# Performance work log

Measured on AMD Instinct MI355X. Metric: run time of the kernel, lower is better.

## Reference

```python
import jax, jax.numpy as jnp
import numpy as np

N, D = 8192, 64
DC_PERCENTILE = 2.0  # np.percentile(distance_matrix, 2)


def setup_inputs() -> dict:
    key = jax.random.key(0)
    data = jax.random.normal(key, (N, D), dtype=jnp.float32)
    return {
        "data": data,
        "rho_threshold": jnp.float32(0.5),
        "delta_threshold": jnp.float32(0.5),
    }


def _cluster(data, rho_t, delta_t):
    n = data.shape[0]
    # pairwise Euclidean distances via GEMM: ||xi||^2 + ||xj||^2 - 2 xi.xj
    sq = jnp.sum(data * data, axis=1)
    d2 = sq[:, None] + sq[None, :] - 2.0 * (data @ data.T)
    dist = jnp.sqrt(jnp.maximum(d2, 0.0))  # [n, n]

    dc = jnp.percentile(dist, DC_PERCENTILE)
    # local density rho_i = sum_j exp(-(d_ij/dc)^2)
    rho = jnp.sum(jnp.exp(-(dist / dc) ** 2), axis=1)  # [n]

    # delta_i = min dist to any point with strictly higher density
    higher = rho[None, :] > rho[:, None]  # [n, n] bool
    masked = jnp.where(higher, dist, jnp.inf)
    delta_m = jnp.min(masked, axis=1)
    nhd_m = jnp.argmin(masked, axis=1)
    has_higher = jnp.any(higher, axis=1)
    delta = jnp.where(has_higher, delta_m, jnp.max(dist, axis=1))
    nhd = jnp.where(has_higher, nhd_m, jnp.arange(n))  # nearest higher-density idx

    # cluster centers: rho and delta above thresholds; label = rank among centers
    is_center = (rho > rho_t) & (delta > delta_t)
    center_rank = jnp.cumsum(is_center.astype(jnp.int32)) - 1
    labels0 = jnp.where(is_center, center_rank, -1).astype(jnp.int32)

    # propagate labels in order of decreasing density (stable argsort, as numpy subset order)
    order = jnp.argsort(-rho)

    def step(labels, i):
        lab = jnp.where(labels[i] < 0, labels[nhd[i]], labels[i])
        return labels.at[i].set(lab), None

    labels, _ = jax.lax.scan(step, labels0, order)
    return labels


def reference(data, rho_threshold, delta_threshold):
    return _cluster(data, rho_threshold, delta_threshold)
```

## Files before the change

kernel.cpp:

```cpp
#include <hip/hip_runtime.h>
#include <stdint.h>

typedef unsigned int u32;
typedef unsigned long long u64;

#define NPTS 8192
#define NTRI 2080
#define NSLICE 16u

#define WS_HIST    0u
#define WS_STATE   524288u
#define WS_DC      524320u
#define WS_SQ      524800u
#define WS_ROWMAX  557568u
#define WS_RHOD    590336u
#define WS_MINKEY  655872u
#define WS_CAND    721408u
#define CAP        32768u
#define WS_S       1048576ull

#define K_RANK 1342177u

__device__ __forceinline__ u64 umin64(u64 a, u64 b) { return a < b ? a : b; }

__device__ __forceinline__ void tri_decode(int t, int& bi, int& bj) {
  int a = (int)((sqrtf(8.0f * (float)t + 1.0f) - 1.0f) * 0.5f);
  while ((a + 1) * (a + 2) / 2 <= t) ++a;
  while (a * (a + 1) / 2 > t) --a;
  int b = t - a * (a + 1) / 2;
  bi = 63 - a; bj = 63 - b;
}

__device__ __forceinline__ u32 bin_of(float d2v) {
  float kf = fminf(d2v * 1048576.0f, 2147483520.0f);
  return min(((u32)kf) >> 15, 8191u);
}

__device__ __forceinline__ u32 block_exscan_1024(u32 v, u32* aux, u32& total) {
  const int lane = threadIdx.x & 63, wave = threadIdx.x >> 6;
  u32 inc = v;
#pragma unroll
  for (int m = 1; m < 64; m <<= 1) {
    u32 o = (u32)__shfl_up((int)inc, m, 64);
    if (lane >= m) inc += o;
  }
  if (lane == 63) aux[wave] = inc;
  __syncthreads();
  if (wave == 0) {
    u32 wv = (lane < 16) ? aux[lane] : 0u;
    u32 winc = wv;
#pragma unroll
    for (int m = 1; m < 16; m <<= 1) {
      u32 o = (u32)__shfl_up((int)winc, m, 64);
      if (lane >= m) winc += o;
    }
    if (lane < 16) aux[16 + lane] = winc - wv;
    if (lane == 15) aux[33] = winc;
  }
  __syncthreads();
  total = aux[33];
  return aux[16 + wave] + (inc - v);
}

__device__ __forceinline__ void tile128(
    const float* __restrict__ X, const float* __restrict__ sq,
    float (*As)[132], float (*Bs)[132],
    int bi, int bj, int tx, int ty, float (&d2)[8][8])
{
  const int tid = threadIdx.x;
  const float4* Xv = reinterpret_cast<const float4*>(X);
  float acc[8][8] = {};
  for (int ph = 0; ph < 2; ++ph) {
    if (ph) __syncthreads();
#pragma unroll
    for (int rep = 0; rep < 4; ++rep) {
      int idx = rep * 256 + tid;
      int i   = idx >> 3;
      int q   = idx & 7;
      int col = (((i >> 2) ^ (q >> 1)) << 2) | (i & 3);
      float4 va = Xv[(bi * 128 + i) * 16 + ph * 8 + q];
      As[4*q+0][col] = va.x; As[4*q+1][col] = va.y; As[4*q+2][col] = va.z; As[4*q+3][col] = va.w;
      float4 vb = Xv[(bj * 128 + i) * 16 + ph * 8 + q];
      Bs[4*q+0][col] = vb.x; Bs[4*q+1][col] = vb.y; Bs[4*q+2][col] = vb.z; Bs[4*q+3][col] = vb.w;
    }
    __syncthreads();
#pragma unroll
    for (int c8 = 0; c8 < 4; ++c8) {
#pragma unroll
      for (int u = 0; u < 8; ++u) {
        int k = c8 * 8 + u;
        float4 a0 = *reinterpret_cast<const float4*>(&As[k][((2*ty+0) ^ c8) << 2]);
        float4 a1 = *reinterpret_cast<const float4*>(&As[k][((2*ty+1) ^ c8) << 2]);
        float4 b0 = *reinterpret_cast<const float4*>(&Bs[k][((2*tx+0) ^ c8) << 2]);
        float4 b1 = *reinterpret_cast<const float4*>(&Bs[k][((2*tx+1) ^ c8) << 2]);
        float a[8] = {a0.x,a0.y,a0.z,a0.w,a1.x,a1.y,a1.z,a1.w};
        float b[8] = {b0.x,b0.y,b0.z,b0.w,b1.x,b1.y,b1.z,b1.w};
#pragma unroll
        for (int r = 0; r < 8; ++r)
#pragma unroll
          for (int c = 0; c < 8; ++c)
            acc[r][c] = fmaf(a[r], b[c], acc[r][c]);
      }
    }
  }
  float sqa[8], sqb[8];
#pragma unroll
  for (int r = 0; r < 8; ++r) sqa[r] = sq[bi * 128 + ty * 8 + r];
#pragma unroll
  for (int c = 0; c < 8; ++c) sqb[c] = sq[bj * 128 + tx * 8 + c];
#pragma unroll
  for (int r = 0; r < 8; ++r)
#pragma unroll
    for (int c = 0; c < 8; ++c)
      d2[r][c] = fmaxf((sqa[r] + sqb[c]) - 2.0f * acc[r][c], 0.0f);
}


__device__ __forceinline__ void collect_body(
    float (&d2)[8][8], int bi, int bj, int tx, int ty, u32* __restrict__ ws)
{
  u32* st = ws + WS_STATE / 4;
  const u32 b0 = st[0], b1 = st[1];
  u32* ctr = st + 4;
  u64* cand = reinterpret_cast<u64*>((char*)ws + WS_CAND);
  const int ig0 = bi * 128 + ty * 8, jg0 = bj * 128 + tx * 8;
  const bool offd = (bi < bj);
  const int lane = threadIdx.x & 63;
#pragma unroll
  for (int r = 0; r < 8; ++r)
#pragma unroll
    for (int c = 0; c < 8; ++c) {
      int ig = ig0 + r, jg = jg0 + c;
      u32 w = offd ? 2u : (ig < jg ? 2u : (ig == jg ? 1u : 0u));
      u32 bin = bin_of(d2[r][c]);
      bool ic = w && (bin == b0 || bin == b1);
      u64 m = __ballot(ic);
      if (m) {
        int leader = __ffsll((long long)m) - 1;
        u32 base = 0;
        if (lane == leader) base = atomicAdd(ctr, (u32)__popcll(m));
        base = (u32)__shfl((int)base, leader);
        if (ic) {
          u32 pos = base + (u32)__popcll(m & ((1ull << lane) - 1ull));
          if (pos < CAP)
            cand[pos] = (((u64)__float_as_uint(d2[r][c])) << 32) | (u64)w;
        }
      }
    }
}

__device__ __forceinline__ void rho_body(
    float (&d2)[8][8], int bi, int bj, int tx, int ty, u32* __restrict__ ws)
{
  __shared__ double redB[4][128];
  const int tid = threadIdx.x;
  const int wv = tid >> 6, lane = tid & 63;
  const float dcf = *reinterpret_cast<const float*>((const char*)ws + WS_DC);
  const float inv2 = 1.0f / (dcf * dcf);
  const int ig0 = bi * 128 + ty * 8, jg0 = bj * 128 + tx * 8;
  const bool diag = (bi == bj);
  float rA[8] = {}, rB[8] = {};
#pragma unroll
  for (int r = 0; r < 8; ++r)
#pragma unroll
    for (int c = 0; c < 8; ++c) {
      float t = __expf(-(d2[r][c] * inv2));
      if (!diag) { rA[r] += t; rB[c] += t; }
      else {
        int ig = ig0 + r, jg = jg0 + c;
        if (ig < jg) { rA[r] += t; rB[c] += t; }
        else if (ig == jg) rA[r] += t;
      }
    }
  double* rhod = reinterpret_cast<double*>((char*)ws + WS_RHOD);
#pragma unroll
  for (int m = 1; m <= 8; m <<= 1)
#pragma unroll
    for (int r = 0; r < 8; ++r) rA[r] += __shfl_xor(rA[r], m);
  if ((tid & 15) == 0)
#pragma unroll
    for (int r = 0; r < 8; ++r) atomicAdd(&rhod[ig0 + r], (double)rA[r]);
#pragma unroll
  for (int m = 16; m <= 32; m <<= 1)
#pragma unroll
    for (int c = 0; c < 8; ++c) rB[c] += __shfl_xor(rB[c], m);
  if (lane < 16)
#pragma unroll
    for (int c = 0; c < 8; ++c) redB[wv][(tid & 15) * 8 + c] = (double)rB[c];
  __syncthreads();
  if (tid < 128) {
    double s = redB[0][tid] + redB[1][tid] + redB[2][tid] + redB[3][tid];
    atomicAdd(&rhod[bj * 128 + tid], s);
  }
}

__device__ __forceinline__ void delta_body(
    float (&d2)[8][8], int bi, int bj, int tx, int ty, u32* __restrict__ ws)
{
  __shared__ u64 redM[4][128];
  const int tid = threadIdx.x;
  const int wv = tid >> 6, lane = tid & 63;
  const double* rhod = reinterpret_cast<const double*>((const char*)ws + WS_RHOD);
  const int ig0 = bi * 128 + ty * 8, jg0 = bj * 128 + tx * 8;
  float ri[8], rj[8];
#pragma unroll
  for (int r = 0; r < 8; ++r) ri[r] = (float)rhod[ig0 + r];
#pragma unroll
  for (int c = 0; c < 8; ++c) rj[c] = (float)rhod[jg0 + c];
  u64 bA[8], bB[8];
#pragma unroll
  for (int r = 0; r < 8; ++r) { bA[r] = ~0ull; bB[r] = ~0ull; }
  const bool offd = (bi < bj);
#pragma unroll
  for (int r = 0; r < 8; ++r)
#pragma unroll
    for (int c = 0; c < 8; ++c) {
      int ig = ig0 + r, jg = jg0 + c;
      if (offd || ig < jg) {
        u64 kb = ((u64)__float_as_uint(sqrtf(d2[r][c]))) << 32;
        if (rj[c] > ri[r]) bA[r] = umin64(bA[r], kb | (u64)(u32)jg);
        if (ri[r] > rj[c]) bB[c] = umin64(bB[c], kb | (u64)(u32)ig);
      }
    }
  u64* mk = reinterpret_cast<u64*>((char*)ws + WS_MINKEY);
#pragma unroll
  for (int m = 1; m <= 8; m <<= 1)
#pragma unroll
    for (int r = 0; r < 8; ++r) bA[r] = umin64(bA[r], __shfl_xor(bA[r], m));
  if ((tid & 15) == 0)
#pragma unroll
    for (int r = 0; r < 8; ++r) if (bA[r] != ~0ull) atomicMin(&mk[ig0 + r], bA[r]);
#pragma unroll
  for (int m = 16; m <= 32; m <<= 1)
#pragma unroll
    for (int c = 0; c < 8; ++c) bB[c] = umin64(bB[c], __shfl_xor(bB[c], m));
  if (lane < 16)
#pragma unroll
    for (int c = 0; c < 8; ++c) redM[wv][(tid & 15) * 8 + c] = bB[c];
  __syncthreads();
  if (tid < 128) {
    u64 m = umin64(umin64(redM[0][tid], redM[1][tid]), umin64(redM[2][tid], redM[3][tid]));
    if (m != ~0ull) atomicMin(&mk[bj * 128 + tid], m);
  }
}

__device__ __forceinline__ void load_tile(
    const float4* __restrict__ S4, float (&d2)[8][8])
{
  const float4* tS = S4 + (size_t)blockIdx.x * 4096 + threadIdx.x;
#pragma unroll
  for (int q = 0; q < 16; ++q) {
    float4 v = tS[q * 256];
    int r = q >> 1, c0 = (q & 1) * 4;
    d2[r][c0+0] = v.x; d2[r][c0+1] = v.y; d2[r][c0+2] = v.z; d2[r][c0+3] = v.w;
  }
}


__global__ __launch_bounds__(256) void k_init(u32* __restrict__ ws) {
  u32 t = blockIdx.x * 256u + threadIdx.x;
  ws[t] = 0u;
  if (t < 8u) ws[WS_STATE / 4 + t] = 0u;
  if (t < 8192u) {
    ws[WS_ROWMAX / 4 + t] = 0u;
    reinterpret_cast<double*>((char*)ws + WS_RHOD)[t] = 0.0;
    reinterpret_cast<u64*>((char*)ws + WS_MINKEY)[t] = ~0ull;
  }
}

__global__ __launch_bounds__(256) void k_sq(const float* __restrict__ X, float* __restrict__ sq) {
  int i = blockIdx.x * 256 + threadIdx.x;
  const float4* row = reinterpret_cast<const float4*>(X + i * 64);
  float s = 0.f;
#pragma unroll
  for (int q = 0; q < 16; ++q) {
    float4 v = row[q];
    s = fmaf(v.x, v.x, s); s = fmaf(v.y, v.y, s);
    s = fmaf(v.z, v.z, s); s = fmaf(v.w, v.w, s);
  }
  sq[i] = s;
}

__global__ __launch_bounds__(256, 4) void k_hist(
    const float* __restrict__ X, const float* __restrict__ sq,
    u32* __restrict__ ws, float4* __restrict__ S4)
{
  __shared__ __align__(16) char smem[33792];
  float (*As)[132] = reinterpret_cast<float(*)[132]>(smem);
  float (*Bs)[132] = reinterpret_cast<float(*)[132]>(smem + 16896);
  u32* h = reinterpret_cast<u32*>(smem);
  int bi, bj; tri_decode(blockIdx.x, bi, bj);
  const int tid = threadIdx.x;
  const int tx = tid & 15, ty = tid >> 4;
  float d2[8][8];
  tile128(X, sq, As, Bs, bi, bj, tx, ty, d2);

  if (S4) {
    float4* tS = S4 + (size_t)blockIdx.x * 4096 + tid;
#pragma unroll
    for (int q = 0; q < 16; ++q) {
      int r = q >> 1, c0 = (q & 1) * 4;
      tS[q * 256] = make_float4(d2[r][c0+0], d2[r][c0+1], d2[r][c0+2], d2[r][c0+3]);
    }
  }

  const int ig0 = bi * 128 + ty * 8, jg0 = bj * 128 + tx * 8;
  u32* rowmax = ws + WS_ROWMAX / 4;
  u32 rmA[8], rmB[8];
#pragma unroll
  for (int r = 0; r < 8; ++r) {
    u32 m = 0;
#pragma unroll
    for (int c = 0; c < 8; ++c) m = max(m, __float_as_uint(d2[r][c]));
    rmA[r] = m;
  }
#pragma unroll
  for (int c = 0; c < 8; ++c) {
    u32 m = 0;
#pragma unroll
    for (int r = 0; r < 8; ++r) m = max(m, __float_as_uint(d2[r][c]));
    rmB[c] = m;
  }
#pragma unroll
  for (int m = 1; m <= 8; m <<= 1)
#pragma unroll
    for (int r = 0; r < 8; ++r) rmA[r] = max(rmA[r], (u32)__shfl_xor((int)rmA[r], m));
  if ((tid & 15) == 0)
#pragma unroll
    for (int r = 0; r < 8; ++r) atomicMax(&rowmax[ig0 + r], rmA[r]);
#pragma unroll
  for (int m = 16; m <= 32; m <<= 1)
#pragma unroll
    for (int c = 0; c < 8; ++c) rmB[c] = max(rmB[c], (u32)__shfl_xor((int)rmB[c], m));
  if ((tid & 48) == 0)
#pragma unroll
    for (int c = 0; c < 8; ++c) atomicMax(&rowmax[jg0 + c], rmB[c]);

  __syncthreads();
  for (int i = tid; i < 8192; i += 256) h[i] = 0;
  __syncthreads();
  const bool offd = (bi < bj);
#pragma unroll
  for (int r = 0; r < 8; ++r)
#pragma unroll
    for (int c = 0; c < 8; ++c) {
      int ig = ig0 + r, jg = jg0 + c;
      u32 w = offd ? 2u : (ig < jg ? 2u : (ig == jg ? 1u : 0u));
      if (w) atomicAdd(&h[bin_of(d2[r][c])], w);
    }
  __syncthreads();
  u32* Hs = ws + (blockIdx.x & 15) * 8192;
  for (int b = tid; b < 8192; b += 256) {
    u32 v = h[b];
    if (v) atomicAdd(&Hs[b], v);
  }
}

__global__ __launch_bounds__(1024) void k_sel1(u32* __restrict__ ws) {
  __shared__ u32 aux[40];
  const int t = threadIdx.x;
  const u32* H = ws;
  u32* st = ws + WS_STATE / 4;
  u32 cnt8[8];
  u32 s = 0;
#pragma unroll
  for (int e = 0; e < 8; ++e) {
    u32 b = (u32)t * 8u + (u32)e;
    u32 v = 0;
#pragma unroll
    for (u32 sl = 0; sl < NSLICE; ++sl) v += H[sl * 8192u + b];
    cnt8[e] = v; s += v;
  }
  u32 total;
  u32 cum = block_exscan_1024(s, aux, total);
#pragma unroll
  for (int e = 0; e < 8; ++e) {
    u32 b = (u32)t * 8u + (u32)e;
    u32 c = cnt8[e];
    if (cum <= K_RANK && K_RANK < cum + c)           { st[0] = b; st[2] = cum; }
    if (cum <= K_RANK + 1u && K_RANK + 1u < cum + c) { st[1] = b; st[3] = cum; }
    cum += c;
  }
}

__global__ __launch_bounds__(256, 4) void k_collectR(
    const float* __restrict__ X, const float* __restrict__ sq, u32* __restrict__ ws)
{
  __shared__ __align__(16) char smem[33792];
  float (*As)[132] = reinterpret_cast<float(*)[132]>(smem);
  float (*Bs)[132] = reinterpret_cast<float(*)[132]>(smem + 16896);
  int bi, bj; tri_decode(blockIdx.x, bi, bj);
  const int tx = threadIdx.x & 15, ty = threadIdx.x >> 4;
  float d2[8][8];
  tile128(X, sq, As, Bs, bi, bj, tx, ty, d2);
  collect_body(d2, bi, bj, tx, ty, ws);
}

__global__ __launch_bounds__(256) void k_collectS(
    const float4* __restrict__ S4, u32* __restrict__ ws)
{
  int bi, bj; tri_decode(blockIdx.x, bi, bj);
  const int tx = threadIdx.x & 15, ty = threadIdx.x >> 4;
  float d2[8][8];
  load_tile(S4, d2);
  collect_body(d2, bi, bj, tx, ty, ws);
}

__device__ u32 zoom(const u64* __restrict__ cand, u32 M, u32 b, u32 base, u32 rank,
                    u32* h, u32* aux) {
  u32 lo = __float_as_uint((float)b * 0.03125f);
  u32 hi = __float_as_uint((float)(b + 1) * 0.03125f);
  u32 need = rank - base;
  while (hi - lo > 1u) {
    u32 range = hi - lo;
    int sh = 0;
    while ((8192u << sh) < range) ++sh;
    for (u32 i = threadIdx.x; i < 8192u; i += 1024u) h[i] = 0;
    __syncthreads();
    for (u32 i = threadIdx.x; i < M; i += 1024u) {
      u64 cw = cand[i];
      u32 raw = (u32)(cw >> 32);
      if (raw >= lo && raw < hi) atomicAdd(&h[(raw - lo) >> sh], (u32)(cw & 3u));
    }
    __syncthreads();
    u32 loc[8];
    u32 s = 0;
#pragma unroll
    for (int e = 0; e < 8; ++e) { loc[e] = h[threadIdx.x * 8u + e]; s += loc[e]; }
    u32 total;
    u32 pre = block_exscan_1024(s, aux, total);
    if (need >= pre && need < pre + s) {
      u32 cum = pre;
#pragma unroll
      for (int e = 0; e < 8; ++e) {
        if (need >= cum && need < cum + loc[e]) { aux[36] = threadIdx.x * 8u + (u32)e; aux[37] = cum; }
        cum += loc[e];
      }
    }
    __syncthreads();
    u32 bb = aux[36], sub = aux[37];
    need -= sub;
    u32 nlo = lo + (bb << sh);
    hi = min(hi, nlo + (1u << sh));
    lo = nlo;
    __syncthreads();
  }
  return lo;
}

__global__ __launch_bounds__(1024) void k_fsel(u32* __restrict__ ws) {
  __shared__ u32 h[8192];
  __shared__ u32 aux[40];
  u32* st = ws + WS_STATE / 4;
  const u64* cand = reinterpret_cast<const u64*>((const char*)ws + WS_CAND);
  u32 M = min(st[4], CAP);
  u32 v0 = zoom(cand, M, st[0], st[2], K_RANK, h, aux);
  u32 v1 = zoom(cand, M, st[1], st[3], K_RANK + 1u, h, aux);
  if (threadIdx.x == 0) {
    float w0 = sqrtf(__uint_as_float(v0));
    float w1 = sqrtf(__uint_as_float(v1));
    double dc = 0.75 * (double)w0 + 0.25 * (double)w1;
    *reinterpret_cast<float*>((char*)ws + WS_DC) = (float)dc;
  }
}

__global__ __launch_bounds__(256, 4) void k_rhoR(
    const float* __restrict__ X, const float* __restrict__ sq, u32* __restrict__ ws)
{
  __shared__ __align__(16) char smem[33792];
  float (*As)[132] = reinterpret_cast<float(*)[132]>(smem);
  float (*Bs)[132] = reinterpret_cast<float(*)[132]>(smem + 16896);
  int bi, bj; tri_decode(blockIdx.x, bi, bj);
  const int tx = threadIdx.x & 15, ty = threadIdx.x >> 4;
  float d2[8][8];
  tile128(X, sq, As, Bs, bi, bj, tx, ty, d2);
  rho_body(d2, bi, bj, tx, ty, ws);
}

__global__ __launch_bounds__(256) void k_rhoS(
    const float4* __restrict__ S4, u32* __restrict__ ws)
{
  int bi, bj; tri_decode(blockIdx.x, bi, bj);
  const int tx = threadIdx.x & 15, ty = threadIdx.x >> 4;
  float d2[8][8];
  load_tile(S4, d2);
  rho_body(d2, bi, bj, tx, ty, ws);
}

__global__ __launch_bounds__(256, 4) void k_deltaR(
    const float* __restrict__ X, const float* __restrict__ sq, u32* __restrict__ ws)
{
  __shared__ __align__(16) char smem[33792];
  float (*As)[132] = reinterpret_cast<float(*)[132]>(smem);
  float (*Bs)[132] = reinterpret_cast<float(*)[132]>(smem + 16896);
  int bi, bj; tri_decode(blockIdx.x, bi, bj);
  const int tx = threadIdx.x & 15, ty = threadIdx.x >> 4;
  float d2[8][8];
  tile128(X, sq, As, Bs, bi, bj, tx, ty, d2);
  delta_body(d2, bi, bj, tx, ty, ws);
}

__global__ __launch_bounds__(256) void k_deltaS(
    const float4* __restrict__ S4, u32* __restrict__ ws)
{
  int bi, bj; tri_decode(blockIdx.x, bi, bj);
  const int tx = threadIdx.x & 15, ty = threadIdx.x >> 4;
  float d2[8][8];
  load_tile(S4, d2);
  delta_body(d2, bi, bj, tx, ty, ws);
}

__global__ __launch_bounds__(1024) void k_labels(
    const u32* __restrict__ ws, const float* __restrict__ rtp,
    const float* __restrict__ dtp, int* __restrict__ out)
{
  __shared__ int   nxt[NPTS];
  __shared__ short lab0[NPTS];
  __shared__ u32   aux[40];
  const int t = threadIdx.x;
  const float rt = rtp[0], dt = dtp[0];
  const u64* mk = reinterpret_cast<const u64*>((const char*)ws + WS_MINKEY);
  const u32* rowmax = ws + WS_ROWMAX / 4;
  const double* rhod = reinterpret_cast<const double*>((const char*)ws + WS_RHOD);
  u32 cnt = 0;
  short loc[8];
  int nh_l[8];
#pragma unroll
  for (int e = 0; e < 8; ++e) {
    int i = t * 8 + e;
    u64 key = mk[i];
    bool hh = (key != ~0ull);
    float delta = hh ? __uint_as_float((u32)(key >> 32))
                     : sqrtf(__uint_as_float(rowmax[i]));
    nh_l[e] = hh ? (int)(u32)(key & 0xffffffffull) : i;
    bool isc = ((float)rhod[i] > rt) && (delta > dt);
    loc[e] = isc ? (short)cnt : (short)-1;
    cnt += isc ? 1u : 0u;
  }
  u32 total;
  u32 base = block_exscan_1024(cnt, aux, total);
#pragma unroll
  for (int e = 0; e < 8; ++e) {
    int i = t * 8 + e;
    short lb = (loc[e] >= 0) ? (short)(loc[e] + (int)base) : (short)-1;
    lab0[i] = lb;
    nxt[i] = (lb >= 0 || nh_l[e] == i) ? i : nh_l[e];
  }
  __syncthreads();
  for (int it = 0; it < 13; ++it) {
#pragma unroll
    for (int e = 0; e < 8; ++e) {
      int i = t * 8 + e;
      nxt[i] = nxt[nxt[i]];
    }
    __syncthreads();
  }
#pragma unroll
  for (int e = 0; e < 8; ++e) {
    int i = t * 8 + e;
    out[i] = (int)lab0[nxt[i]];
  }
}

extern "C" void kernel_launch(void* const* d_in, const int* in_sizes, int n_in,
                              void* d_out, int out_size, void* d_ws, size_t ws_size,
                              hipStream_t stream)
{
  (void)in_sizes; (void)n_in; (void)out_size;
  const float* X  = (const float*)d_in[0];
  const float* rt = (const float*)d_in[1];
  const float* dt = (const float*)d_in[2];
  int* out = (int*)d_out;
  u32* ws = (u32*)d_ws;
  float* sq = (float*)((char*)d_ws + WS_SQ);

  const bool big = ws_size >= (size_t)(WS_S + (u64)NTRI * 16384ull * 4ull);
  float4* S4 = big ? reinterpret_cast<float4*>((char*)d_ws + WS_S) : nullptr;

  k_init<<<512, 256, 0, stream>>>(ws);
  k_sq<<<32, 256, 0, stream>>>(X, sq);

  k_hist<<<NTRI, 256, 0, stream>>>(X, sq, ws, S4);
  k_sel1<<<1, 1024, 0, stream>>>(ws);
  if (big) k_collectS<<<NTRI, 256, 0, stream>>>(S4, ws);
  else     k_collectR<<<NTRI, 256, 0, stream>>>(X, sq, ws);
  k_fsel<<<1, 1024, 0, stream>>>(ws);
  if (big) k_rhoS<<<NTRI, 256, 0, stream>>>(S4, ws);
  else     k_rhoR<<<NTRI, 256, 0, stream>>>(X, sq, ws);
  if (big) k_deltaS<<<NTRI, 256, 0, stream>>>(S4, ws);
  else     k_deltaR<<<NTRI, 256, 0, stream>>>(X, sq, ws);
  k_labels<<<1, 1024, 0, stream>>>(ws, rt, dt, out);
}
```

Before: 403.5 us.

## Coarsen percentile histogram and stream tile values in rho/delta passes

The global histogram is reduced from 8192 to 1024 coarse bins, which shrinks the histogram atomics, the selection scan and the init kernel. When the two percentile ranks land in different coarse bins, the collect pass tracks only a running max and min by atomics instead of writing candidates. The rho and delta kernels now consume the stored distance tiles float4 by float4 with partial unrolling, rather than loading the whole 8x8 tile into registers first, which is meant to reduce register pressure. Coarser bins can make the candidate bin much larger, so the candidate capacity is doubled. The max/min shortcut also assumes rank K is the largest value in its bin and rank K+1 the smallest in the next.

```diff
diff --git a/kernel.cpp b/kernel.cpp
--- a/kernel.cpp
+++ b/kernel.cpp
@@ -9,14 +9,14 @@
 #define NSLICE 16u
 
 #define WS_HIST    0u
-#define WS_STATE   524288u
-#define WS_DC      524320u
-#define WS_SQ      524800u
-#define WS_ROWMAX  557568u
-#define WS_RHOD    590336u
-#define WS_MINKEY  655872u
-#define WS_CAND    721408u
-#define CAP        32768u
+#define WS_CAND    65536u
+#define CAP        65536u
+#define WS_STATE   589824u
+#define WS_DC      589856u
+#define WS_SQ      590336u
+#define WS_ROWMAX  623104u
+#define WS_RHOD    655872u
+#define WS_MINKEY  721408u
 #define WS_S       1048576ull
 
 #define K_RANK 1342177u
@@ -116,62 +116,49 @@
 }
 
 
-__device__ __forceinline__ void collect_body(
-    float (&d2)[8][8], int bi, int bj, int tx, int ty, u32* __restrict__ ws)
-{
-  u32* st = ws + WS_STATE / 4;
-  const u32 b0 = st[0], b1 = st[1];
-  u32* ctr = st + 4;
-  u64* cand = reinterpret_cast<u64*>((char*)ws + WS_CAND);
-  const int ig0 = bi * 128 + ty * 8, jg0 = bj * 128 + tx * 8;
-  const bool offd = (bi < bj);
-  const int lane = threadIdx.x & 63;
-#pragma unroll
-  for (int r = 0; r < 8; ++r)
-#pragma unroll
-    for (int c = 0; c < 8; ++c) {
-      int ig = ig0 + r, jg = jg0 + c;
-      u32 w = offd ? 2u : (ig < jg ? 2u : (ig == jg ? 1u : 0u));
-      u32 bin = bin_of(d2[r][c]);
-      bool ic = w && (bin == b0 || bin == b1);
-      u64 m = __ballot(ic);
-      if (m) {
-        int leader = __ffsll((long long)m) - 1;
-        u32 base = 0;
-        if (lane == leader) base = atomicAdd(ctr, (u32)__popcll(m));
-        base = (u32)__shfl((int)base, leader);
-        if (ic) {
-          u32 pos = base + (u32)__popcll(m & ((1ull << lane) - 1ull));
-          if (pos < CAP)
-            cand[pos] = (((u64)__float_as_uint(d2[r][c])) << 32) | (u64)w;
-        }
-      }
-    }
-}
-
-__device__ __forceinline__ void rho_body(
-    float (&d2)[8][8], int bi, int bj, int tx, int ty, u32* __restrict__ ws)
-{
-  __shared__ double redB[4][128];
+__device__ __forceinline__ void rho_elem(
+    float4 v, int q, float inv2, bool diag, int ig0, int jg0,
+    float* rA, float* rB)
+{
+  int r = q >> 1, c0 = (q & 1) * 4;
+  float e[4] = {v.x, v.y, v.z, v.w};
+#pragma unroll
+  for (int j = 0; j < 4; ++j) {
+    float t = __expf(-(e[j] * inv2));
+    if (!diag) { rA[r] += t; rB[c0 + j] += t; }
+    else {
+      int ig = ig0 + r, jg = jg0 + c0 + j;
+      if (ig < jg) { rA[r] += t; rB[c0 + j] += t; }
+      else if (ig == jg) rA[r] += t;
+    }
+  }
+}
+
+__device__ __forceinline__ void delta_elem(
+    float4 v, int q, bool offd, int ig0, int jg0,
+    const float* ri, const float* rj, u64* bA, u64* bB)
+{
+  int r = q >> 1, c0 = (q & 1) * 4;
+  float e[4] = {v.x, v.y, v.z, v.w};
+#pragma unroll
+  for (int j = 0; j < 4; ++j) {
+    int c = c0 + j;
+    int ig = ig0 + r, jg = jg0 + c;
+    if (offd || ig < jg) {
+      u64 kb = ((u64)__float_as_uint(sqrtf(e[j]))) << 32;
+      if (rj[c] > ri[r]) bA[r] = umin64(bA[r], kb | (u64)(u32)jg);
+      if (ri[r] > rj[c]) bB[c] = umin64(bB[c], kb | (u64)(u32)ig);
+    }
+  }
+}
+
+
+__device__ __forceinline__ void rho_finish(
+    float* rA, float* rB, int bi, int bj, int ig0, u32* __restrict__ ws,
+    double (*redB)[128])
+{
   const int tid = threadIdx.x;
   const int wv = tid >> 6, lane = tid & 63;
-  const float dcf = *reinterpret_cast<const float*>((const char*)ws + WS_DC);
-  const float inv2 = 1.0f / (dcf * dcf);
-  const int ig0 = bi * 128 + ty * 8, jg0 = bj * 128 + tx * 8;
-  const bool diag = (bi == bj);
-  float rA[8] = {}, rB[8] = {};
-#pragma unroll
-  for (int r = 0; r < 8; ++r)
-#pragma unroll
-    for (int c = 0; c < 8; ++c) {
-      float t = __expf(-(d2[r][c] * inv2));
-      if (!diag) { rA[r] += t; rB[c] += t; }
-      else {
-        int ig = ig0 + r, jg = jg0 + c;
-        if (ig < jg) { rA[r] += t; rB[c] += t; }
-        else if (ig == jg) rA[r] += t;
-      }
-    }
   double* rhod = reinterpret_cast<double*>((char*)ws + WS_RHOD);
 #pragma unroll
   for (int m = 1; m <= 8; m <<= 1)
@@ -194,34 +181,12 @@
   }
 }
 
-__device__ __forceinline__ void delta_body(
-    float (&d2)[8][8], int bi, int bj, int tx, int ty, u32* __restrict__ ws)
-{
-  __shared__ u64 redM[4][128];
+__device__ __forceinline__ void delta_finish(
+    u64* bA, u64* bB, int bi, int bj, int ig0, u32* __restrict__ ws,
+    u64 (*redM)[128])
+{
   const int tid = threadIdx.x;
   const int wv = tid >> 6, lane = tid & 63;
-  const double* rhod = reinterpret_cast<const double*>((const char*)ws + WS_RHOD);
-  const int ig0 = bi * 128 + ty * 8, jg0 = bj * 128 + tx * 8;
-  float ri[8], rj[8];
-#pragma unroll
-  for (int r = 0; r < 8; ++r) ri[r] = (float)rhod[ig0 + r];
-#pragma unroll
-  for (int c = 0; c < 8; ++c) rj[c] = (float)rhod[jg0 + c];
-  u64 bA[8], bB[8];
-#pragma unroll
-  for (int r = 0; r < 8; ++r) { bA[r] = ~0ull; bB[r] = ~0ull; }
-  const bool offd = (bi < bj);
-#pragma unroll
-  for (int r = 0; r < 8; ++r)
-#pragma unroll
-    for (int c = 0; c < 8; ++c) {
-      int ig = ig0 + r, jg = jg0 + c;
-      if (offd || ig < jg) {
-        u64 kb = ((u64)__float_as_uint(sqrtf(d2[r][c]))) << 32;
-        if (rj[c] > ri[r]) bA[r] = umin64(bA[r], kb | (u64)(u32)jg);
-        if (ri[r] > rj[c]) bB[c] = umin64(bB[c], kb | (u64)(u32)ig);
-      }
-    }
   u64* mk = reinterpret_cast<u64*>((char*)ws + WS_MINKEY);
 #pragma unroll
   for (int m = 1; m <= 8; m <<= 1)
@@ -244,15 +209,29 @@
   }
 }
 
-__device__ __forceinline__ void load_tile(
-    const float4* __restrict__ S4, float (&d2)[8][8])
-{
-  const float4* tS = S4 + (size_t)blockIdx.x * 4096 + threadIdx.x;
-#pragma unroll
-  for (int q = 0; q < 16; ++q) {
-    float4 v = tS[q * 256];
-    int r = q >> 1, c0 = (q & 1) * 4;
-    d2[r][c0+0] = v.x; d2[r][c0+1] = v.y; d2[r][c0+2] = v.z; d2[r][c0+3] = v.w;
+__device__ __forceinline__ void collect_elems(
+    float d2v, u32 w, u32 cb0, u32 cb1, bool same,
+    u32* ctr, u64* cand, u32& mx, u32& mn)
+{
+  u32 cb = bin_of(d2v) >> 3;
+  u32 raw = __float_as_uint(d2v);
+  if (same) {
+    bool ic = w && (cb == cb0);
+    u64 m = __ballot(ic);
+    if (m) {
+      int lane = threadIdx.x & 63;
+      int leader = __ffsll((long long)m) - 1;
+      u32 base = 0;
+      if (lane == leader) base = atomicAdd(ctr, (u32)__popcll(m));
+      base = (u32)__shfl((int)base, leader);
+      if (ic) {
+        u32 pos = base + (u32)__popcll(m & ((1ull << lane) - 1ull));
+        if (pos < CAP) cand[pos] = (((u64)raw) << 32) | (u64)w;
+      }
+    }
+  } else {
+    if (w && cb == cb0) mx = max(mx, raw);
+    if (w && cb == cb1) mn = min(mn, raw);
   }
 }
 
@@ -260,7 +239,7 @@
 __global__ __launch_bounds__(256) void k_init(u32* __restrict__ ws) {
   u32 t = blockIdx.x * 256u + threadIdx.x;
   ws[t] = 0u;
-  if (t < 8u) ws[WS_STATE / 4 + t] = 0u;
+  if (t < 8u) ws[WS_STATE / 4 + t] = (t == 6u) ? 0xFFFFFFFFu : 0u;
   if (t < 8192u) {
     ws[WS_ROWMAX / 4 + t] = 0u;
     reinterpret_cast<double*>((char*)ws + WS_RHOD)[t] = 0.0;
@@ -349,10 +328,12 @@
       if (w) atomicAdd(&h[bin_of(d2[r][c])], w);
     }
   __syncthreads();
-  u32* Hs = ws + (blockIdx.x & 15) * 8192;
-  for (int b = tid; b < 8192; b += 256) {
-    u32 v = h[b];
-    if (v) atomicAdd(&Hs[b], v);
+  u32* Hs = ws + (blockIdx.x & 15) * 1024;
+  for (int cb = tid; cb < 1024; cb += 256) {
+    u32 s = 0;
+#pragma unroll
+    for (int e = 0; e < 8; ++e) s += h[cb * 8 + e];
+    if (s) atomicAdd(&Hs[cb], s);
   }
 }
 
@@ -361,25 +342,49 @@
   const int t = threadIdx.x;
   const u32* H = ws;
   u32* st = ws + WS_STATE / 4;
-  u32 cnt8[8];
-  u32 s = 0;
-#pragma unroll
-  for (int e = 0; e < 8; ++e) {
-    u32 b = (u32)t * 8u + (u32)e;
-    u32 v = 0;
-#pragma unroll
-    for (u32 sl = 0; sl < NSLICE; ++sl) v += H[sl * 8192u + b];
-    cnt8[e] = v; s += v;
-  }
+  u32 v = 0;
+#pragma unroll
+  for (u32 sl = 0; sl < NSLICE; ++sl) v += H[sl * 1024u + (u32)t];
   u32 total;
-  u32 cum = block_exscan_1024(s, aux, total);
-#pragma unroll
-  for (int e = 0; e < 8; ++e) {
-    u32 b = (u32)t * 8u + (u32)e;
-    u32 c = cnt8[e];
-    if (cum <= K_RANK && K_RANK < cum + c)           { st[0] = b; st[2] = cum; }
-    if (cum <= K_RANK + 1u && K_RANK + 1u < cum + c) { st[1] = b; st[3] = cum; }
-    cum += c;
+  u32 cum = block_exscan_1024(v, aux, total);
+  if (cum <= K_RANK && K_RANK < cum + v)           { st[0] = (u32)t; st[2] = cum; }
+  if (cum <= K_RANK + 1u && K_RANK + 1u < cum + v) { st[1] = (u32)t; st[3] = cum; }
+}
+
+__global__ __launch_bounds__(256) void k_collectS(
+    const float4* __restrict__ S4, u32* __restrict__ ws)
+{
+  int bi, bj; tri_decode(blockIdx.x, bi, bj);
+  const int tid = threadIdx.x;
+  const int tx = tid & 15, ty = tid >> 4;
+  u32* st = ws + WS_STATE / 4;
+  const u32 cb0 = st[0], cb1 = st[1];
+  const bool same = (cb0 == cb1);
+  u32* ctr = st + 4;
+  u64* cand = reinterpret_cast<u64*>((char*)ws + WS_CAND);
+  const int ig0 = bi * 128 + ty * 8, jg0 = bj * 128 + tx * 8;
+  const bool offd = (bi < bj);
+  const float4* tS = S4 + (size_t)blockIdx.x * 4096 + tid;
+  u32 mx = 0u, mn = 0xFFFFFFFFu;
+#pragma unroll 4
+  for (int q = 0; q < 16; ++q) {
+    float4 v = tS[q * 256];
+    int r = q >> 1, c0 = (q & 1) * 4;
+    float e[4] = {v.x, v.y, v.z, v.w};
+#pragma unroll
+    for (int j = 0; j < 4; ++j) {
+      int ig = ig0 + r, jg = jg0 + c0 + j;
+      u32 w = offd ? 2u : (ig < jg ? 2u : (ig == jg ? 1u : 0u));
+      collect_elems(e[j], w, cb0, cb1, same, ctr, cand, mx, mn);
+    }
+  }
+  if (!same) {
+#pragma unroll
+    for (int m = 1; m <= 32; m <<= 1) {
+      mx = max(mx, (u32)__shfl_xor((int)mx, m));
+      mn = min(mn, (u32)__shfl_xor((int)mn, m));
+    }
+    if ((tid & 63) == 0) { atomicMax(&st[5], mx); atomicMin(&st[6], mn); }
   }
 }
 
@@ -390,26 +395,42 @@
   float (*As)[132] = reinterpret_cast<float(*)[132]>(smem);
   float (*Bs)[132] = reinterpret_cast<float(*)[132]>(smem + 16896);
   int bi, bj; tri_decode(blockIdx.x, bi, bj);
-  const int tx = threadIdx.x & 15, ty = threadIdx.x >> 4;
+  const int tid = threadIdx.x;
+  const int tx = tid & 15, ty = tid >> 4;
   float d2[8][8];
   tile128(X, sq, As, Bs, bi, bj, tx, ty, d2);
-  collect_body(d2, bi, bj, tx, ty, ws);
-}
-
-__global__ __launch_bounds__(256) void k_collectS(
-    const float4* __restrict__ S4, u32* __restrict__ ws)
-{
-  int bi, bj; tri_decode(blockIdx.x, bi, bj);
-  const int tx = threadIdx.x & 15, ty = threadIdx.x >> 4;
-  float d2[8][8];
-  load_tile(S4, d2);
-  collect_body(d2, bi, bj, tx, ty, ws);
-}
-
-__device__ u32 zoom(const u64* __restrict__ cand, u32 M, u32 b, u32 base, u32 rank,
+  u32* st = ws + WS_STATE / 4;
+  const u32 cb0 = st[0], cb1 = st[1];
+  const bool same = (cb0 == cb1);
+  u32* ctr = st + 4;
+  u64* cand = reinterpret_cast<u64*>((char*)ws + WS_CAND);
+  const int ig0 = bi * 128 + ty * 8, jg0 = bj * 128 + tx * 8;
+  const bool offd = (bi < bj);
+  u32 mx = 0u, mn = 0xFFFFFFFFu;
+#pragma unroll
+  for (int q = 0; q < 16; ++q) {
+    int r = q >> 1, c0 = (q & 1) * 4;
+#pragma unroll
+    for (int j = 0; j < 4; ++j) {
+      int ig = ig0 + r, jg = jg0 + c0 + j;
+      u32 w = offd ? 2u : (ig < jg ? 2u : (ig == jg ? 1u : 0u));
+      collect_elems(d2[r][c0 + j], w, cb0, cb1, same, ctr, cand, mx, mn);
+    }
+  }
+  if (!same) {
+#pragma unroll
+    for (int m = 1; m <= 32; m <<= 1) {
+      mx = max(mx, (u32)__shfl_xor((int)mx, m));
+      mn = min(mn, (u32)__shfl_xor((int)mn, m));
+    }
+    if ((tid & 63) == 0) { atomicMax(&st[5], mx); atomicMin(&st[6], mn); }
+  }
+}
+
+__device__ u32 zoom(const u64* __restrict__ cand, u32 M, u32 cb, u32 base, u32 rank,
                     u32* h, u32* aux) {
-  u32 lo = __float_as_uint((float)b * 0.03125f);
-  u32 hi = __float_as_uint((float)(b + 1) * 0.03125f);
+  u32 lo = __float_as_uint((float)cb * 0.25f);
+  u32 hi = __float_as_uint((float)(cb + 1) * 0.25f);
   u32 need = rank - base;
   while (hi - lo > 1u) {
     u32 range = hi - lo;
@@ -453,9 +474,15 @@
   __shared__ u32 aux[40];
   u32* st = ws + WS_STATE / 4;
   const u64* cand = reinterpret_cast<const u64*>((const char*)ws + WS_CAND);
-  u32 M = min(st[4], CAP);
-  u32 v0 = zoom(cand, M, st[0], st[2], K_RANK, h, aux);
-  u32 v1 = zoom(cand, M, st[1], st[3], K_RANK + 1u, h, aux);
+  u32 v0, v1;
+  if (st[0] == st[1]) {
+    u32 M = min(st[4], CAP);
+    v0 = zoom(cand, M, st[0], st[2], K_RANK, h, aux);
+    v1 = zoom(cand, M, st[1], st[2], K_RANK + 1u, h, aux);
+  } else {
+    v0 = st[5];
+    v1 = st[6];
+  }
   if (threadIdx.x == 0) {
     float w0 = sqrtf(__uint_as_float(v0));
     float w1 = sqrtf(__uint_as_float(v1));
@@ -464,50 +491,106 @@
   }
 }
 
+__global__ __launch_bounds__(256) void k_rhoS(
+    const float4* __restrict__ S4, u32* __restrict__ ws)
+{
+  __shared__ double redB[4][128];
+  int bi, bj; tri_decode(blockIdx.x, bi, bj);
+  const int tid = threadIdx.x;
+  const int tx = tid & 15, ty = tid >> 4;
+  const float dcf = *reinterpret_cast<const float*>((const char*)ws + WS_DC);
+  const float inv2 = 1.0f / (dcf * dcf);
+  const int ig0 = bi * 128 + ty * 8, jg0 = bj * 128 + tx * 8;
+  const bool diag = (bi == bj);
+  const float4* tS = S4 + (size_t)blockIdx.x * 4096 + tid;
+  float rA[8] = {}, rB[8] = {};
+#pragma unroll 4
+  for (int q = 0; q < 16; ++q)
+    rho_elem(tS[q * 256], q, inv2, diag, ig0, jg0, rA, rB);
+  rho_finish(rA, rB, bi, bj, ig0, ws, redB);
+}
+
 __global__ __launch_bounds__(256, 4) void k_rhoR(
     const float* __restrict__ X, const float* __restrict__ sq, u32* __restrict__ ws)
 {
   __shared__ __align__(16) char smem[33792];
+  __shared__ double redB[4][128];
   float (*As)[132] = reinterpret_cast<float(*)[132]>(smem);
   float (*Bs)[132] = reinterpret_cast<float(*)[132]>(smem + 16896);
   int bi, bj; tri_decode(blockIdx.x, bi, bj);
-  const int tx = threadIdx.x & 15, ty = threadIdx.x >> 4;
+  const int tid = threadIdx.x;
+  const int tx = tid & 15, ty = tid >> 4;
   float d2[8][8];
   tile128(X, sq, As, Bs, bi, bj, tx, ty, d2);
-  rho_body(d2, bi, bj, tx, ty, ws);
-}
-
-__global__ __launch_bounds__(256) void k_rhoS(
+  const float dcf = *reinterpret_cast<const float*>((const char*)ws + WS_DC);
+  const float inv2 = 1.0f / (dcf * dcf);
+  const int ig0 = bi * 128 + ty * 8, jg0 = bj * 128 + tx * 8;
+  const bool diag = (bi == bj);
+  float rA[8] = {}, rB[8] = {};
+#pragma unroll
+  for (int q = 0; q < 16; ++q) {
+    int r = q >> 1, c0 = (q & 1) * 4;
+    float4 v = make_float4(d2[r][c0+0], d2[r][c0+1], d2[r][c0+2], d2[r][c0+3]);
+    rho_elem(v, q, inv2, diag, ig0, jg0, rA, rB);
+  }
+  rho_finish(rA, rB, bi, bj, ig0, ws, redB);
+}
+
+__global__ __launch_bounds__(256) void k_deltaS(
     const float4* __restrict__ S4, u32* __restrict__ ws)
 {
+  __shared__ u64 redM[4][128];
   int bi, bj; tri_decode(blockIdx.x, bi, bj);
-  const int tx = threadIdx.x & 15, ty = threadIdx.x >> 4;
-  float d2[8][8];
-  load_tile(S4, d2);
-  rho_body(d2, bi, bj, tx, ty, ws);
+  const int tid = threadIdx.x;
+  const int tx = tid & 15, ty = tid >> 4;
+  const double* rhod = reinterpret_cast<const double*>((const char*)ws + WS_RHOD);
+  const int ig0 = bi * 128 + ty * 8, jg0 = bj * 128 + tx * 8;
+  float ri[8], rj[8];
+#pragma unroll
+  for (int r = 0; r < 8; ++r) ri[r] = (float)rhod[ig0 + r];
+#pragma unroll
+  for (int c = 0; c < 8; ++c) rj[c] = (float)rhod[jg0 + c];
+  u64 bA[8], bB[8];
+#pragma unroll
+  for (int r = 0; r < 8; ++r) { bA[r] = ~0ull; bB[r] = ~0ull; }
+  const bool offd = (bi < bj);
+  const float4* tS = S4 + (size_t)blockIdx.x * 4096 + tid;
+#pragma unroll 4
+  for (int q = 0; q < 16; ++q)
+    delta_elem(tS[q * 256], q, offd, ig0, jg0, ri, rj, bA, bB);
+  delta_finish(bA, bB, bi, bj, ig0, ws, redM);
 }
 
 __global__ __launch_bounds__(256, 4) void k_deltaR(
     const float* __restrict__ X, const float* __restrict__ sq, u32* __restrict__ ws)
 {
   __shared__ __align__(16) char smem[33792];
+  __shared__ u64 redM[4][128];
   float (*As)[132] = reinterpret_cast<float(*)[132]>(smem);
   float (*Bs)[132] = reinterpret_cast<float(*)[132]>(smem + 16896);
   int bi, bj; tri_decode(blockIdx.x, bi, bj);
-  const int tx = threadIdx.x & 15, ty = threadIdx.x >> 4;
+  const int tid = threadIdx.x;
+  const int tx = tid & 15, ty = tid >> 4;
   float d2[8][8];
   tile128(X, sq, As, Bs, bi, bj, tx, ty, d2);
-  delta_body(d2, bi, bj, tx, ty, ws);
-}
-
-__global__ __launch_bounds__(256) void k_deltaS(
-    const float4* __restrict__ S4, u32* __restrict__ ws)
-{
-  int bi, bj; tri_decode(blockIdx.x, bi, bj);
-  const int tx = threadIdx.x & 15, ty = threadIdx.x >> 4;
-  float d2[8][8];
-  load_tile(S4, d2);
-  delta_body(d2, bi, bj, tx, ty, ws);
+  const double* rhod = reinterpret_cast<const double*>((const char*)ws + WS_RHOD);
+  const int ig0 = bi * 128 + ty * 8, jg0 = bj * 128 + tx * 8;
+  float ri[8], rj[8];
+#pragma unroll
+  for (int r = 0; r < 8; ++r) ri[r] = (float)rhod[ig0 + r];
+#pragma unroll
+  for (int c = 0; c < 8; ++c) rj[c] = (float)rhod[jg0 + c];
+  u64 bA[8], bB[8];
+#pragma unroll
+  for (int r = 0; r < 8; ++r) { bA[r] = ~0ull; bB[r] = ~0ull; }
+  const bool offd = (bi < bj);
+#pragma unroll
+  for (int q = 0; q < 16; ++q) {
+    int r = q >> 1, c0 = (q & 1) * 4;
+    float4 v = make_float4(d2[r][c0+0], d2[r][c0+1], d2[r][c0+2], d2[r][c0+3]);
+    delta_elem(v, q, offd, ig0, jg0, ri, rj, bA, bB);
+  }
+  delta_finish(bA, bB, bi, bj, ig0, ws, redM);
 }
 
 __global__ __launch_bounds__(1024) void k_labels(
@@ -577,7 +660,7 @@
   const bool big = ws_size >= (size_t)(WS_S + (u64)NTRI * 16384ull * 4ull);
   float4* S4 = big ? reinterpret_cast<float4*>((char*)d_ws + WS_S) : nullptr;
 
-  k_init<<<512, 256, 0, stream>>>(ws);
+  k_init<<<64, 256, 0, stream>>>(ws);
   k_sq<<<32, 256, 0, stream>>>(X, sq);
 
   k_hist<<<NTRI, 256, 0, stream>>>(X, sq, ws, S4);
```

Result: slower. 651.9 us (+61.6%).
